# Performance work log

Measured on AMD Instinct MI355X. Metric: run time of the kernel, lower is better.

## Reference

```python
import jax, jax.numpy as jnp
import numpy as np

N = 100_000      # nodes
E = 1_600_000    # edges (avg degree 16)
IN_DIM = 165
HIDDEN = 64
OUT_DIM = 2


def setup_inputs() -> dict:
    key = jax.random.key(0)
    ks = jax.random.split(key, 10)
    x = jax.random.normal(ks[0], (N, IN_DIM), dtype=jnp.float32)
    edge_index = jax.random.randint(ks[1], (2, E), 0, N, dtype=jnp.int32)
    def lin(k, fan_in, fan_out):
        lim = 1.0 / np.sqrt(fan_in)
        return jax.random.uniform(k, (fan_in, fan_out), jnp.float32, -lim, lim)
    # SAGEConv: lin_l (neighbor path, with bias), lin_r (root path, no bias)
    W1l = lin(ks[2], IN_DIM, HIDDEN); b1 = jnp.zeros((HIDDEN,), jnp.float32)
    W1r = lin(ks[3], IN_DIM, HIDDEN)
    W2l = lin(ks[4], HIDDEN, HIDDEN); b2 = jnp.zeros((HIDDEN,), jnp.float32)
    W2r = lin(ks[5], HIDDEN, HIDDEN)
    Wc = lin(ks[6], HIDDEN, OUT_DIM)
    bc = jax.random.uniform(ks[7], (OUT_DIM,), jnp.float32, -0.1, 0.1)
    return {"x": x, "edge_index": edge_index, "W1l": W1l, "b1": b1, "W1r": W1r,
            "W2l": W2l, "b2": b2, "W2r": W2r, "Wc": Wc, "bc": bc}


def _sage_conv(h, src, dst, Wl, bl, Wr):
    # mean-aggregate source features at destination nodes, then two linears
    msg = h[src]                                              # [E, D] gather
    agg = jax.ops.segment_sum(msg, dst, num_segments=N)       # [N, D] scatter-add
    cnt = jax.ops.segment_sum(jnp.ones((src.shape[0], 1), h.dtype), dst,
                              num_segments=N)                 # [N, 1] in-degree
    mean = agg / jnp.maximum(cnt, 1.0)
    return mean @ Wl + bl + h @ Wr


def reference(x, edge_index, W1l, b1, W1r, W2l, b2, W2r, Wc, bc):
    src, dst = edge_index[0], edge_index[1]
    h = jax.nn.relu(_sage_conv(x, src, dst, W1l, b1, W1r))
    # dropout is a no-op at inference (training=False)
    h = jax.nn.relu(_sage_conv(h, src, dst, W2l, b2, W2r))
    return h @ Wc + bc
```

## Files before the change

### kernel.cpp

```cpp
#include <hip/hip_runtime.h>
#include <hip/hip_fp16.h>
#include <cstdint>

#define NN 100000
#define NE 1600000
#define INDIM 165
#define HID 64
#define KP1 192
#define KP2 64

constexpr int BSH = 7;
constexpr int BNODES = 128;
constexpr int NBUK = (NN + BNODES - 1) / BNODES;
constexpr int SC_CHUNK = 8192;
constexpr int BCAP = 2816;

typedef _Float16 f16x8 __attribute__((ext_vector_type(8)));
typedef _Float16 h2 __attribute__((ext_vector_type(2)));
typedef float f32x4 __attribute__((ext_vector_type(4)));

__device__ __forceinline__ void gload16(const float* g, float* l) {
    __builtin_amdgcn_global_load_lds(
        (const __attribute__((address_space(1))) uint32_t*)g,
        (__attribute__((address_space(3))) uint32_t*)l, 16, 0, 0);
}


__global__ __launch_bounds__(256) void k_bscan(const int* __restrict__ bcnt,
                                               int* __restrict__ bbase) {
    __shared__ int wsum[4];
    const int tid = threadIdx.x, lane = tid & 63, wid = tid >> 6;
    int v[4];
    int tsum = 0;
#pragma unroll
    for (int i = 0; i < 4; ++i) {
        int idx = tid * 4 + i;
        v[i] = (idx < NBUK) ? bcnt[idx] : 0;
        tsum += v[i];
    }
    int x = tsum;
#pragma unroll
    for (int off = 1; off < 64; off <<= 1) {
        int y = __shfl_up(x, off, 64);
        if (lane >= off) x += y;
    }
    if (lane == 63) wsum[wid] = x;
    __syncthreads();
    int woff = 0;
#pragma unroll
    for (int w = 0; w < 4; ++w)
        if (w < wid) woff += wsum[w];
    int run = woff + x - tsum;
#pragma unroll
    for (int i = 0; i < 4; ++i) {
        int idx = tid * 4 + i;
        if (idx < NBUK) bbase[idx] = run;
        run += v[i];
    }
    if (tid == 255) bbase[NBUK] = woff + x;
}


__global__ __launch_bounds__(256) void k_scatter(const int* __restrict__ src,
                                                 const int* __restrict__ dst,
                                                 int* __restrict__ bcnt,
                                                 unsigned* __restrict__ Eb, int ne) {
    __shared__ int hist[NBUK];
    __shared__ int base[NBUK];
    const int tid = threadIdx.x;
    const int cs = blockIdx.x * SC_CHUNK;
    for (int b = tid; b < NBUK; b += 256) hist[b] = 0;
    __syncthreads();
    unsigned pack[SC_CHUNK / 256];
#pragma unroll 8
    for (int i = 0; i < SC_CHUNK / 256; ++i) {
        int e = cs + i * 256 + tid;
        if (e < ne) {
            int b = dst[e] >> BSH;
            int r = atomicAdd(&hist[b], 1);
            pack[i] = (unsigned)((b << 13) | r);
        } else {
            pack[i] = 0xFFFFFFFFu;
        }
    }
    __syncthreads();
    for (int b = tid; b < NBUK; b += 256) {
        int c = hist[b];
        base[b] = c ? atomicAdd(&bcnt[b], c) : 0;
    }
    __syncthreads();
#pragma unroll 8
    for (int i = 0; i < SC_CHUNK / 256; ++i) {
        if (pack[i] != 0xFFFFFFFFu) {
            int e = cs + i * 256 + tid;
            int b = pack[i] >> 13, r = pack[i] & 8191;
            int pos = base[b] + r;
            if (pos < BCAP)
                Eb[(size_t)b * BCAP + pos] =
                    (unsigned)src[e] | ((unsigned)(dst[e] & (BNODES - 1)) << 17);
        }
    }
}


__global__ __launch_bounds__(256) void k_csrb(const unsigned* __restrict__ Eb,
                                              const int* __restrict__ bbase,
                                              int* __restrict__ rowptr,
                                              int* __restrict__ col, int n) {
    __shared__ int cnt[BNODES];
    __shared__ int pref[BNODES];
    const int tid = threadIdx.x;
    const int gb = bbase[blockIdx.x];
    const int m = bbase[blockIdx.x + 1] - gb;
    const unsigned* eb = Eb + (size_t)blockIdx.x * BCAP;
    for (int i = tid; i < BNODES; i += 256) cnt[i] = 0;
    __syncthreads();
    for (int e = tid; e < m; e += 256)
        atomicAdd(&cnt[eb[e] >> 17], 1);
    __syncthreads();
    if (tid < 64) {
        int c0 = cnt[tid * 2], c1 = cnt[tid * 2 + 1];
        int s = c0 + c1;
        int x = s;
#pragma unroll
        for (int off = 1; off < 64; off <<= 1) {
            int y = __shfl_up(x, off, 64);
            if (tid >= off) x += y;
        }
        int ex = x - s;
        pref[tid * 2] = ex;
        pref[tid * 2 + 1] = ex + c0;
    }
    __syncthreads();
    const int nodeBase = blockIdx.x * BNODES;
    for (int i = tid; i < BNODES; i += 256) {
        int gn = nodeBase + i;
        if (gn < n) rowptr[gn] = gb + pref[i];
        cnt[i] = 0;
    }
    __syncthreads();
    for (int e = tid; e < m; e += 256) {
        unsigned v = eb[e];
        int d = (int)(v >> 17);
        int r = atomicAdd(&cnt[d], 1);
        col[gb + pref[d] + r] = (int)(v & 0x1FFFFu);
    }
    if (blockIdx.x == 0 && tid == 0) rowptr[n] = bbase[NBUK];
}


__global__ __launch_bounds__(256) void k_wcvt(const float* __restrict__ W1l,
                                              const float* __restrict__ W1r,
                                              const float* __restrict__ W2l,
                                              const float* __restrict__ W2r,
                                              _Float16* __restrict__ Wt1,
                                              _Float16* __restrict__ Wt2) {
    int o = blockIdx.x * 256 + threadIdx.x;
    if (o < 128 * KP1) {
        int c = o / KP1, k = o - c * KP1;
        float v = 0.f;
        if (k < INDIM) v = (c < HID) ? W1l[k * HID + c] : W1r[k * HID + (c - HID)];
        Wt1[o] = (_Float16)v;
    } else if (o < 128 * KP1 + 128 * KP2) {
        int p = o - 128 * KP1;
        int c = p / KP2, k = p - c * KP2;
        float v = (c < HID) ? W2l[k * HID + c] : W2r[k * HID + (c - HID)];
        Wt2[p] = (_Float16)v;
    }
}


__global__ __launch_bounds__(256) void k_lin1(const float* __restrict__ X,
                                              const _Float16* __restrict__ Wt,
                                              _Float16* __restrict__ Y,
                                              _Float16* __restrict__ Rh, int n) {
    constexpr int ROWD = INDIM;
    constexpr int LDSZ = 64 * 168;
    __shared__ float Xs[LDSZ];
    const int tid = threadIdx.x;
    const int lane = tid & 63;
    const int wi = tid >> 6;
    const int jn = lane & 15;
    const int kq = lane >> 4;
    const int r0 = blockIdx.x * 64;
    const int vr = (n - r0 < 64) ? (n - r0) : 64;
    const int cnt = vr * ROWD;
    const int nFull = cnt >> 8;
    const float* __restrict__ P = X + (size_t)r0 * ROWD;

    for (int i = cnt + tid; i < cnt + 192 && i < LDSZ; i += 256) Xs[i] = 0.f;

    for (int i = wi; i < nFull; i += 4)
        gload16(P + i * 256 + lane * 4, Xs + i * 256);
    for (int i = (nFull << 8) + tid; i < cnt; i += 256) Xs[i] = P[i];
    __syncthreads();

    const _Float16* wp = Wt + (size_t)jn * KP1 + kq * 8;
    const float* xrow = &Xs[(wi * 16 + jn) * ROWD + kq * 8];

    f32x4 acc[8];
#pragma unroll
    for (int t = 0; t < 8; ++t) acc[t] = (f32x4){0.f, 0.f, 0.f, 0.f};

#pragma unroll
    for (int c = 0; c < 6; ++c) {
        f16x8 xb;
#pragma unroll
        for (int j = 0; j < 8; ++j) xb[j] = (_Float16)xrow[c * 32 + j];
#pragma unroll
        for (int t = 0; t < 8; ++t) {
            const f16x8 wa = *(const f16x8*)(wp + t * (16 * KP1) + c * 32);
            acc[t] = __builtin_amdgcn_mfma_f32_16x16x32_f16(wa, xb, acc[t], 0, 0, 0);
        }
    }

    const int gn0 = r0 + wi * 16 + jn;
    if (gn0 < n) {
#pragma unroll
        for (int t = 0; t < 8; ++t) {
            const int cb = (t & 3) * 16 + kq * 4;
            union { _Float16 h[4]; uint2 u; } u;
#pragma unroll
            for (int r = 0; r < 4; ++r) u.h[r] = (_Float16)acc[t][r];
            _Float16* dstp = (t < 4) ? (Y + (size_t)gn0 * HID + cb)
                                     : (Rh + (size_t)gn0 * HID + cb);
            *(uint2*)dstp = u.u;
        }
    }
}


template <int KPAD>
__global__ __launch_bounds__(256, 4) void k_linear(const _Float16* __restrict__ Xh,
                                                   const _Float16* __restrict__ Wt,
                                                   _Float16* __restrict__ Y,
                                                   _Float16* __restrict__ Rh, int n) {
    const int tid = threadIdx.x;
    const int lane = tid & 63;
    const int w = tid >> 6;
    const int jn = lane & 15;
    const int kq = lane >> 4;
    const int gn0 = blockIdx.x * 64 + w * 16 + jn;
    const int gn = (gn0 < n) ? gn0 : (n - 1);

    const _Float16* xp = Xh + (size_t)gn * KPAD + kq * 8;
    const _Float16* wp = Wt + (size_t)jn * KPAD + kq * 8;

    f16x8 xf[KPAD / 32];
#pragma unroll
    for (int c = 0; c < KPAD / 32; ++c)
        xf[c] = *(const f16x8*)(xp + c * 32);

    f32x4 acc[8];
#pragma unroll
    for (int t = 0; t < 8; ++t) acc[t] = (f32x4){0.f, 0.f, 0.f, 0.f};

#pragma unroll
    for (int c = 0; c < KPAD / 32; ++c) {
#pragma unroll
        for (int t = 0; t < 8; ++t) {
            const f16x8 wa = *(const f16x8*)(wp + t * (16 * KPAD) + c * 32);
            acc[t] = __builtin_amdgcn_mfma_f32_16x16x32_f16(wa, xf[c], acc[t], 0, 0, 0);
        }
    }

    if (gn0 < n) {
#pragma unroll
        for (int t = 0; t < 8; ++t) {
            const int cb = (t & 3) * 16 + kq * 4;
            union { _Float16 h[4]; uint2 u; } u;
#pragma unroll
            for (int r = 0; r < 4; ++r) u.h[r] = (_Float16)acc[t][r];
            _Float16* dstp = (t < 4) ? (Y + (size_t)gn * HID + cb)
                                     : (Rh + (size_t)gn * HID + cb);
            *(uint2*)dstp = u.u;
        }
    }
}


__device__ __forceinline__ void acc2(float& ax, float& ay, h2 v) {
    ax += (float)v[0];
    ay += (float)v[1];
}

template <bool CLS>
__global__ __launch_bounds__(256) void k_agg(const _Float16* __restrict__ Y,
                                             const _Float16* __restrict__ Rm,
                                             const float* __restrict__ bias,
                                             const int* __restrict__ rowptr,
                                             const int* __restrict__ col,
                                             _Float16* __restrict__ H,
                                             const float* __restrict__ Wc,
                                             const float* __restrict__ bc,
                                             float* __restrict__ out, int n) {
    const int lane = threadIdx.x & 63;
    const int node = blockIdx.x * 4 + (threadIdx.x >> 6);
    if (node >= n) return;
    const int half_ = lane >> 5;
    const unsigned fp = (unsigned)(lane & 31);
    const h2* __restrict__ Y2 = (const h2*)Y;
    const int s = rowptr[node], e = rowptr[node + 1];
    float ax0 = 0.f, ay0 = 0.f, ax1 = 0.f, ay1 = 0.f;
    int i = s + half_;
    for (; i + 14 < e; i += 16) {
        int c[8];
#pragma unroll
        for (int j = 0; j < 8; ++j) c[j] = col[i + 2 * j];
        h2 y[8];
#pragma unroll
        for (int j = 0; j < 8; ++j) y[j] = Y2[(unsigned)c[j] * 32u + fp];
#pragma unroll
        for (int j = 0; j < 8; j += 2) {
            acc2(ax0, ay0, y[j]);
            acc2(ax1, ay1, y[j + 1]);
        }
    }
    for (; i + 6 < e; i += 8) {
        int c[4];
#pragma unroll
        for (int j = 0; j < 4; ++j) c[j] = col[i + 2 * j];
        h2 y[4];
#pragma unroll
        for (int j = 0; j < 4; ++j) y[j] = Y2[(unsigned)c[j] * 32u + fp];
        acc2(ax0, ay0, y[0]);
        acc2(ax1, ay1, y[1]);
        acc2(ax0, ay0, y[2]);
        acc2(ax1, ay1, y[3]);
    }
    for (; i < e; i += 2)
        acc2(ax0, ay0, Y2[(unsigned)col[i] * 32u + fp]);
    float ax = ax0 + ax1, ay = ay0 + ay1;
    ax += __shfl_xor(ax, 32, 64);
    ay += __shfl_xor(ay, 32, 64);
    const float vx = __shfl(ax, lane >> 1, 64);
    const float vy = __shfl(ay, lane >> 1, 64);
    const float acc = (lane & 1) ? vy : vx;
    const int deg = e - s;
    float h = acc / (float)(deg > 1 ? deg : 1) + bias[lane] +
              (float)Rm[(size_t)node * HID + lane];
    h = fmaxf(h, 0.f);
    if (!CLS) {
        H[(size_t)node * HID + lane] = (_Float16)h;
    } else {
        float p0 = h * Wc[lane * 2 + 0];
        float p1 = h * Wc[lane * 2 + 1];
#pragma unroll
        for (int off = 32; off > 0; off >>= 1) {
            p0 += __shfl_xor(p0, off, 64);
            p1 += __shfl_xor(p1, off, 64);
        }
        if (lane == 0) {
            out[(size_t)node * 2 + 0] = p0 + bc[0];
            out[(size_t)node * 2 + 1] = p1 + bc[1];
        }
    }
}


extern "C" void kernel_launch(void* const* d_in, const int* in_sizes, int n_in,
                              void* d_out, int out_size, void* d_ws, size_t ws_size,
                              hipStream_t stream) {
    const float* x   = (const float*)d_in[0];
    const int*   ei  = (const int*)d_in[1];
    const float* W1l = (const float*)d_in[2];
    const float* b1  = (const float*)d_in[3];
    const float* W1r = (const float*)d_in[4];
    const float* W2l = (const float*)d_in[5];
    const float* b2  = (const float*)d_in[6];
    const float* W2r = (const float*)d_in[7];
    const float* Wc  = (const float*)d_in[8];
    const float* bc  = (const float*)d_in[9];
    float* out = (float*)d_out;
    const int* src = ei;
    const int* dst = ei + NE;

    char* base = (char*)d_ws;
    size_t off = 0;
    auto alloc = [&](size_t bytes) {
        void* p = base + off;
        off = (off + bytes + 255) & ~(size_t)255;
        return p;
    };
    int*      bcnt    = (int*)alloc((size_t)NBUK * 4);
    int*      bbase   = (int*)alloc((size_t)(NBUK + 1) * 4);
    int*      rowptr  = (int*)alloc((size_t)(NN + 1) * 4);
    int*      col     = (int*)alloc((size_t)NE * 4);
    _Float16* Y       = (_Float16*)alloc((size_t)NN * HID * 2 + 256);
    _Float16* Rh      = (_Float16*)alloc((size_t)NN * HID * 2);
    _Float16* Hh      = (_Float16*)alloc((size_t)NN * HID * 2);
    _Float16* Wt1     = (_Float16*)alloc((size_t)128 * KP1 * 2);
    _Float16* Wt2     = (_Float16*)alloc((size_t)128 * KP2 * 2);
    unsigned* Eb      = (unsigned*)Y;

    const int sb = (NE + SC_CHUNK - 1) / SC_CHUNK;
    const int wb = (128 * KP1 + 128 * KP2 + 255) / 256;

    hipMemsetAsync(bcnt, 0, (size_t)NBUK * 4, stream);
    k_scatter<<<sb, 256, 0, stream>>>(src, dst, bcnt, Eb, NE);
    k_bscan<<<1, 256, 0, stream>>>(bcnt, bbase);
    k_csrb<<<NBUK, 256, 0, stream>>>(Eb, bbase, rowptr, col, NN);
    k_wcvt<<<wb, 256, 0, stream>>>(W1l, W1r, W2l, W2r, Wt1, Wt2);

    k_lin1<<<(NN + 63) / 64, 256, 0, stream>>>(x, Wt1, Y, Rh, NN);
    k_agg<false><<<(NN + 3) / 4, 256, 0, stream>>>(Y, Rh, b1, rowptr, col, Hh,
                                                   nullptr, nullptr, nullptr, NN);
    k_linear<KP2><<<(NN + 63) / 64, 256, 0, stream>>>(Hh, Wt2, Y, Rh, NN);
    k_agg<true><<<(NN + 3) / 4, 256, 0, stream>>>(Y, Rh, b2, rowptr, col, nullptr,
                                                  Wc, bc, out, NN);
}
```

Baseline: 324.7 us.

## Fuse weight conversion into bucket scan, per-wave X staging, fp16 pairwise aggregation

Folds the weight transpose/convert kernel into the bucket-scan launch as extra blocks, removing one kernel launch. In the first linear layer, each wave now stages only its own 16 rows of X into LDS and waits on its own loads instead of a block barrier; padding zeros are replaced by masking the last K chunk. The aggregation kernel sums neighbour features pairwise in fp16 before converting to fp32, cutting conversions but adding rounding error in half precision.

```diff
diff --git a/kernel.cpp b/kernel.cpp
--- a/kernel.cpp
+++ b/kernel.cpp
@@ -27,7 +27,28 @@
 
 
 __global__ __launch_bounds__(256) void k_bscan(const int* __restrict__ bcnt,
-                                               int* __restrict__ bbase) {
+                                               int* __restrict__ bbase,
+                                               const float* __restrict__ W1l,
+                                               const float* __restrict__ W1r,
+                                               const float* __restrict__ W2l,
+                                               const float* __restrict__ W2r,
+                                               _Float16* __restrict__ Wt1,
+                                               _Float16* __restrict__ Wt2) {
+    if (blockIdx.x > 0) {
+        int o = (blockIdx.x - 1) * 256 + threadIdx.x;
+        if (o < 128 * KP1) {
+            int c = o / KP1, k = o - c * KP1;
+            float v = 0.f;
+            if (k < INDIM) v = (c < HID) ? W1l[k * HID + c] : W1r[k * HID + (c - HID)];
+            Wt1[o] = (_Float16)v;
+        } else if (o < 128 * KP1 + 128 * KP2) {
+            int p = o - 128 * KP1;
+            int c = p / KP2, k = p - c * KP2;
+            float v = (c < HID) ? W2l[k * HID + c] : W2r[k * HID + (c - HID)];
+            Wt2[p] = (_Float16)v;
+        }
+        return;
+    }
     __shared__ int wsum[4];
     const int tid = threadIdx.x, lane = tid & 63, wid = tid >> 6;
     int v[4];
@@ -149,34 +170,12 @@
 }
 
 
-__global__ __launch_bounds__(256) void k_wcvt(const float* __restrict__ W1l,
-                                              const float* __restrict__ W1r,
-                                              const float* __restrict__ W2l,
-                                              const float* __restrict__ W2r,
-                                              _Float16* __restrict__ Wt1,
-                                              _Float16* __restrict__ Wt2) {
-    int o = blockIdx.x * 256 + threadIdx.x;
-    if (o < 128 * KP1) {
-        int c = o / KP1, k = o - c * KP1;
-        float v = 0.f;
-        if (k < INDIM) v = (c < HID) ? W1l[k * HID + c] : W1r[k * HID + (c - HID)];
-        Wt1[o] = (_Float16)v;
-    } else if (o < 128 * KP1 + 128 * KP2) {
-        int p = o - 128 * KP1;
-        int c = p / KP2, k = p - c * KP2;
-        float v = (c < HID) ? W2l[k * HID + c] : W2r[k * HID + (c - HID)];
-        Wt2[p] = (_Float16)v;
-    }
-}
-
-
 __global__ __launch_bounds__(256) void k_lin1(const float* __restrict__ X,
                                               const _Float16* __restrict__ Wt,
                                               _Float16* __restrict__ Y,
                                               _Float16* __restrict__ Rh, int n) {
-    constexpr int ROWD = INDIM;
-    constexpr int LDSZ = 64 * 168;
-    __shared__ float Xs[LDSZ];
+    constexpr int WROWD = 16 * INDIM;
+    __shared__ float Xs[4 * WROWD];
     const int tid = threadIdx.x;
     const int lane = tid & 63;
     const int wi = tid >> 6;
@@ -184,19 +183,24 @@
     const int kq = lane >> 4;
     const int r0 = blockIdx.x * 64;
     const int vr = (n - r0 < 64) ? (n - r0) : 64;
-    const int cnt = vr * ROWD;
-    const int nFull = cnt >> 8;
-    const float* __restrict__ P = X + (size_t)r0 * ROWD;
-
-    for (int i = cnt + tid; i < cnt + 192 && i < LDSZ; i += 256) Xs[i] = 0.f;
-
-    for (int i = wi; i < nFull; i += 4)
-        gload16(P + i * 256 + lane * 4, Xs + i * 256);
-    for (int i = (nFull << 8) + tid; i < cnt; i += 256) Xs[i] = P[i];
-    __syncthreads();
-
+    const int cnt = vr * INDIM;
+    const float* __restrict__ P = X + (size_t)r0 * INDIM;
+
+    const int myS = wi * WROWD;
+    int d = cnt - myS;
+    if (d > WROWD) d = WROWD;
+    if (d > 0) {
+        const int nd = d >> 8;
+        for (int i = 0; i < nd; ++i)
+            gload16(P + myS + i * 256 + lane * 4, Xs + myS + i * 256);
+        for (int i = myS + (nd << 8) + lane; i < myS + d; i += 64)
+            Xs[i] = P[i];
+        asm volatile("s_waitcnt vmcnt(0)" ::: "memory");
+        __builtin_amdgcn_sched_barrier(0);
+    }
+
+    const float* xrow = &Xs[(wi * 16 + jn) * INDIM + kq * 8];
     const _Float16* wp = Wt + (size_t)jn * KP1 + kq * 8;
-    const float* xrow = &Xs[(wi * 16 + jn) * ROWD + kq * 8];
 
     f32x4 acc[8];
 #pragma unroll
@@ -205,8 +209,14 @@
 #pragma unroll
     for (int c = 0; c < 6; ++c) {
         f16x8 xb;
-#pragma unroll
-        for (int j = 0; j < 8; ++j) xb[j] = (_Float16)xrow[c * 32 + j];
+        if (c < 5) {
+#pragma unroll
+            for (int j = 0; j < 8; ++j) xb[j] = (_Float16)xrow[c * 32 + j];
+        } else {
+#pragma unroll
+            for (int j = 0; j < 8; ++j)
+                xb[j] = (kq == 0 && j < 5) ? (_Float16)xrow[160 + j] : (_Float16)0.f;
+        }
 #pragma unroll
         for (int t = 0; t < 8; ++t) {
             const f16x8 wa = *(const f16x8*)(wp + t * (16 * KP1) + c * 32);
@@ -278,11 +288,6 @@
     }
 }
 
-
-__device__ __forceinline__ void acc2(float& ax, float& ay, h2 v) {
-    ax += (float)v[0];
-    ay += (float)v[1];
-}
 
 template <bool CLS>
 __global__ __launch_bounds__(256) void k_agg(const _Float16* __restrict__ Y,
@@ -310,11 +315,10 @@
         h2 y[8];
 #pragma unroll
         for (int j = 0; j < 8; ++j) y[j] = Y2[(unsigned)c[j] * 32u + fp];
-#pragma unroll
-        for (int j = 0; j < 8; j += 2) {
-            acc2(ax0, ay0, y[j]);
-            acc2(ax1, ay1, y[j + 1]);
-        }
+        h2 b0 = (y[0] + y[1]) + (y[2] + y[3]);
+        h2 b1 = (y[4] + y[5]) + (y[6] + y[7]);
+        ax0 += (float)b0[0]; ay0 += (float)b0[1];
+        ax1 += (float)b1[0]; ay1 += (float)b1[1];
     }
     for (; i + 6 < e; i += 8) {
         int c[4];
@@ -323,13 +327,13 @@
         h2 y[4];
 #pragma unroll
         for (int j = 0; j < 4; ++j) y[j] = Y2[(unsigned)c[j] * 32u + fp];
-        acc2(ax0, ay0, y[0]);
-        acc2(ax1, ay1, y[1]);
-        acc2(ax0, ay0, y[2]);
-        acc2(ax1, ay1, y[3]);
-    }
-    for (; i < e; i += 2)
-        acc2(ax0, ay0, Y2[(unsigned)col[i] * 32u + fp]);
+        h2 b0 = (y[0] + y[1]) + (y[2] + y[3]);
+        ax0 += (float)b0[0]; ay0 += (float)b0[1];
+    }
+    for (; i < e; i += 2) {
+        h2 v = Y2[(unsigned)col[i] * 32u + fp];
+        ax0 += (float)v[0]; ay0 += (float)v[1];
+    }
     float ax = ax0 + ax1, ay = ay0 + ay1;
     ax += __shfl_xor(ax, 32, 64);
     ay += __shfl_xor(ay, 32, 64);
@@ -394,13 +398,12 @@
     unsigned* Eb      = (unsigned*)Y;
 
     const int sb = (NE + SC_CHUNK - 1) / SC_CHUNK;
-    const int wb = (128 * KP1 + 128 * KP2 + 255) / 256;
+    const int wb = 1 + (128 * KP1 + 128 * KP2 + 255) / 256;
 
     hipMemsetAsync(bcnt, 0, (size_t)NBUK * 4, stream);
     k_scatter<<<sb, 256, 0, stream>>>(src, dst, bcnt, Eb, NE);
-    k_bscan<<<1, 256, 0, stream>>>(bcnt, bbase);
+    k_bscan<<<wb, 256, 0, stream>>>(bcnt, bbase, W1l, W1r, W2l, W2r, Wt1, Wt2);
     k_csrb<<<NBUK, 256, 0, stream>>>(Eb, bbase, rowptr, col, NN);
-    k_wcvt<<<wb, 256, 0, stream>>>(W1l, W1r, W2l, W2r, Wt1, Wt2);
 
     k_lin1<<<(NN + 63) / 64, 256, 0, stream>>>(x, Wt1, Y, Rh, NN);
     k_agg<false><<<(NN + 3) / 4, 256, 0, stream>>>(Y, Rh, b1, rowptr, col, Hh,
```

Result: no change. 324.7 us (-0.0%).
